# Kernel optimization log

Measured on AMD Instinct MI355X. Metric: run time of the kernel, lower is better.

Reference implementation:

```python
import jax, jax.numpy as jnp
import numpy as np

COMMITMENT_COST = 0.25
DECAY = 0.99
EPSILON = 1e-05


def setup_inputs() -> dict:
    key = jax.random.key(0)
    k1, k2, k3, k4 = jax.random.split(key, 4)
    S, B, D, K = 256, 64, 512, 4096
    return {
        "inputs": jax.random.normal(k1, (S, B, D), dtype=jnp.float32),
        "embedding_weight": jax.random.normal(k2, (K, D), dtype=jnp.float32),
        "ema_w": jax.random.normal(k3, (K, D), dtype=jnp.float32),
        "ema_cluster_size": jax.random.uniform(k4, (K,), dtype=jnp.float32),
    }


def reference(inputs, embedding_weight, ema_w, ema_cluster_size):
    S, B, D = inputs.shape
    K = embedding_weight.shape[0]
    flat = inputs.reshape(-1, D)  # [N, D], N = S*B

    distances = (
        jnp.sum(flat * flat, axis=1, keepdims=True)
        + jnp.sum(embedding_weight * embedding_weight, axis=1)
        - 2.0 * flat @ embedding_weight.T
    )
    encoding_indices = jnp.argmin(distances, axis=1)  # [N]
    encodings = jax.nn.one_hot(encoding_indices, K, dtype=inputs.dtype)  # [N, K]

    # gather codebook rows (equivalent to encodings @ weight)
    quantized = jnp.take(embedding_weight, encoding_indices, axis=0).reshape(S, B, D)
    encodings_flat = encodings.reshape(S, B, K)

    # EMA codebook update (training-mode buffers; computed with stop_gradient semantics)
    counts = jnp.sum(encodings, axis=0)  # [K]
    new_cluster_size = ema_cluster_size * DECAY + (1.0 - DECAY) * counts
    n = jnp.sum(new_cluster_size)
    new_cluster_size = (new_cluster_size + EPSILON) / (n + K * EPSILON) * n
    dw = jax.ops.segment_sum(flat, encoding_indices, num_segments=K)  # encodings.T @ flat
    new_ema_w = ema_w * DECAY + (1.0 - DECAY) * dw
    new_embedding_weight = new_ema_w / new_cluster_size[:, None]

    # commitment loss (quantized detached)
    e_latent_loss = jnp.mean((jax.lax.stop_gradient(quantized) - inputs) ** 2)
    loss = COMMITMENT_COST * e_latent_loss

    # straight-through estimator
    quantized_st = inputs + jax.lax.stop_gradient(quantized - inputs)

    return (
        loss,
        quantized_st,
        encodings_flat,
        encoding_indices[:, None],
        new_embedding_weight,
        new_cluster_size,
        new_ema_w,
    )
```

## Files before the change

kernel.cpp:

```cpp
#include <hip/hip_runtime.h>
#include <hip/hip_bf16.h>
#include <cstdint>
#include <cstddef>

typedef __attribute__((ext_vector_type(8))) short short8;
typedef __attribute__((ext_vector_type(4))) float f32x4;
typedef __attribute__((ext_vector_type(4))) unsigned int u32x4;

#define D_DIM 512
#define K_DIM 4096
#define N_ROWS 16384

#define DECAY_F 0.99f
#define OMD_F 0.01f
#define EPS_F 1e-5f
#define COMMIT_F 0.25f
#define MARGIN_F 0.75f

#define OFF_LOSS 0
#define OFF_QST 1
#define OFF_ENC (1 + 8388608)
#define OFF_IDX (OFF_ENC + 67108864)
#define OFF_NEW_W (OFF_IDX + 16384)
#define OFF_NEW_CS (OFF_NEW_W + 2097152)
#define OFF_NEW_EMA (OFF_NEW_CS + 4096)

#define WS_MINKEY 0
#define WS_COUNTS 131072
#define WS_E2 147456
#define WS_LOSSP 163840
#define WS_RCNT 164096
#define WS_ARENA 164112

#define AR_M1K 0
#define AR_M2V 4194304
#define AR_XHI 6291456
#define AR_EHI 23068672
#define AR_RROW 27262976
#define AR_RCUT 27328512
#define AR_NEED 27394048
#define WS_NEED (WS_ARENA + AR_NEED)

#define SCR0 8388612

__device__ __forceinline__ unsigned long long mkkey(float d, int c) {
  unsigned u = __float_as_uint(d);
  u ^= (unsigned)(((int)u) >> 31) | 0x80000000u;
  return ((unsigned long long)u << 32) | (unsigned)c;
}
__device__ __forceinline__ float keyval(unsigned long long k) {
  unsigned u = (unsigned)(k >> 32);
  u = (u & 0x80000000u) ? (u ^ 0x80000000u) : ~u;
  return __uint_as_float(u);
}
__device__ __forceinline__ void merge2(unsigned long long& k1, float& v2,
                                       unsigned long long ko, float v2o) {
  float v1 = keyval(k1), v1o = keyval(ko);
  float vmax = fmaxf(v1, v1o);
  v2 = fminf(fminf(v2, v2o), vmax);
  if (ko < k1) k1 = ko;
}
__device__ __forceinline__ unsigned pk2o(float a, float b) {
  unsigned ua = (__float_as_uint(a) + 0x8000u) & 0xFFFF0000u;
  unsigned ub = (__float_as_uint(b) + 0x8000u) & 0xFFFF0000u;
  return (ua >> 16) | ub;
}
__device__ __forceinline__ void gl_lds16(const void* g, void* l) {
  __builtin_amdgcn_global_load_lds(
      (const __attribute__((address_space(1))) unsigned int*)g,
      (__attribute__((address_space(3))) unsigned int*)l, 16, 0, 0);
}

__global__ void k_e2(const float* __restrict__ E, float* __restrict__ e2,
                     uint4* __restrict__ ehi, int* __restrict__ counts,
                     float* __restrict__ loss_part, int* __restrict__ rcnt) {
  int tid = threadIdx.x;
  int lane = tid & 63;
  int w = tid >> 6;
  int k = blockIdx.x * 4 + w;
  if (tid < 4) counts[blockIdx.x * 4 + tid] = 0;
  if (blockIdx.x == 0 && tid < 64) loss_part[tid] = 0.f;
  if (blockIdx.x == 1 && tid == 0) *rcnt = 0;
  const float4* ev = (const float4*)(E + (size_t)k * D_DIM);
  float4 a = ev[lane * 2], b = ev[lane * 2 + 1];
  uint4 h;
  h.x = pk2o(a.x, a.y);
  h.y = pk2o(a.z, a.w);
  h.z = pk2o(b.x, b.y);
  h.w = pk2o(b.z, b.w);
  ehi[(size_t)k * 64 + lane] = h;
  float s = a.x * a.x + a.y * a.y + a.z * a.z + a.w * a.w +
            b.x * b.x + b.y * b.y + b.z * b.z + b.w * b.w;
#pragma unroll
  for (int off = 32; off > 0; off >>= 1) s += __shfl_down(s, off, 64);
  if (lane == 0) e2[k] = s;
}

__global__ void k_conv(const float* __restrict__ src, uint4* __restrict__ hi) {
  int t = blockIdx.x * 256 + threadIdx.x;
  const float4* s4 = (const float4*)src;
  float4 a = s4[t * 2], b = s4[t * 2 + 1];
  uint4 h;
  h.x = pk2o(a.x, a.y);
  h.y = pk2o(a.z, a.w);
  h.z = pk2o(b.x, b.y);
  h.w = pk2o(b.z, b.w);
  hi[t] = h;
}

__global__ void k_scale_emaw(const float* __restrict__ ema_w, float* __restrict__ out) {
  int i = blockIdx.x * 256 + threadIdx.x;
  out[OFF_NEW_EMA + i] = DECAY_F * ema_w[i];
}

__global__ __launch_bounds__(256, 2) void k_gemm(
    const char* __restrict__ xhi, const char* __restrict__ ehi,
    const float* __restrict__ e2, unsigned long long* __restrict__ m1k,
    float* __restrict__ m2v) {
  extern __shared__ char smem[];
  const int tid = threadIdx.x;
  const int w = tid >> 6, lane = tid & 63;
  const int wr = w >> 1, wc = w & 1;
  const int l15 = lane & 15, g = lane >> 4;
  const int row0 = blockIdx.x * 128;
  const int col0 = blockIdx.y * 128;

  const char* srcBase = (w < 2) ? xhi : ehi;
  const int srcRow0 = (w < 2) ? (row0 + 64 * w) : (col0 + 64 * (w - 2));
  const int lr = lane >> 3;
  const int lc = lane & 7;
  const char* srcLane = srcBase + (size_t)(srcRow0 + lr) * 1024 + ((lc ^ lr) << 4);
  const int dstOff = w * 8192;

#define STAGE(c, b)                                       \
  {                                                       \
    const char* sp_ = srcLane + (c) * 128;                \
    char* lb_ = smem + (b) * 32768 + dstOff;              \
    _Pragma("unroll") for (int q = 0; q < 8; ++q)         \
        gl_lds16(sp_ + q * 8192, lb_ + q * 1024);         \
  }

  f32x4 acc[4][4];
  const f32x4 z = {0.f, 0.f, 0.f, 0.f};
#pragma unroll
  for (int i = 0; i < 4; ++i)
#pragma unroll
    for (int j = 0; j < 4; ++j) acc[i][j] = z;

  STAGE(0, 0);
  const int s0 = (g ^ (l15 & 7)) << 4;
  const int aRow = (wr * 64 + l15) * 128;
  const int bRow = (wc * 64 + l15) * 128;

  for (int c = 0; c < 8; ++c) {
    __syncthreads();
    if (c < 7) STAGE(c + 1, (c + 1) & 1);
    const char* Ab = smem + (c & 1) * 32768;
    const char* Bb = Ab + 16384;
    short8 a[2][4], b[2][4];
#pragma unroll
    for (int kk = 0; kk < 2; ++kk) {
      const int sw = s0 ^ (kk << 6);
#pragma unroll
      for (int i = 0; i < 4; ++i) {
        a[kk][i] = *(const short8*)(Ab + aRow + i * 2048 + sw);
        b[kk][i] = *(const short8*)(Bb + bRow + i * 2048 + sw);
      }
    }
#pragma unroll
    for (int kk = 0; kk < 2; ++kk)
#pragma unroll
      for (int i = 0; i < 4; ++i)
#pragma unroll
        for (int j = 0; j < 4; ++j)
          acc[i][j] = __builtin_amdgcn_mfma_f32_16x16x32_bf16(a[kk][i], b[kk][j], acc[i][j], 0, 0, 0);
  }
#undef STAGE

  __syncthreads();
  unsigned long long* lk = (unsigned long long*)smem;
  float* lv = (float*)(smem + 2048);
  float e2v[4];
#pragma unroll
  for (int j = 0; j < 4; ++j) e2v[j] = e2[col0 + wc * 64 + j * 16 + l15];

#pragma unroll
  for (int i = 0; i < 4; ++i) {
    int rowl = wr * 64 + i * 16 + (g << 2);
#pragma unroll
    for (int r = 0; r < 4; ++r) {
      unsigned long long k1 = 0;
      float v2 = 3.4e38f;
#pragma unroll
      for (int j = 0; j < 4; ++j) {
        float dv = fmaf(-2.f, acc[i][j][r], e2v[j]);
        unsigned long long kk = mkkey(dv, col0 + wc * 64 + j * 16 + l15);
        if (j == 0) k1 = kk;
        else merge2(k1, v2, kk, 3.4e38f);
      }
#pragma unroll
      for (int m = 1; m <= 8; m <<= 1) {
        unsigned long long ko = __shfl_xor(k1, m, 64);
        float vo = __shfl_xor(v2, m, 64);
        merge2(k1, v2, ko, vo);
      }
      if (l15 == 0) {
        lk[(rowl + r) * 2 + wc] = k1;
        lv[(rowl + r) * 2 + wc] = v2;
      }
    }
  }
  __syncthreads();
  if (tid < 128) {
    unsigned long long k1 = lk[tid * 2];
    float v2 = lv[tid * 2];
    merge2(k1, v2, lk[tid * 2 + 1], lv[tid * 2 + 1]);
    size_t o = (size_t)(row0 + tid) * 32 + blockIdx.y;
    m1k[o] = k1;
    m2v[o] = v2;
  }
}

__global__ void k_reduce(const unsigned long long* __restrict__ m1k,
                         const float* __restrict__ m2v,
                         unsigned long long* __restrict__ minkey,
                         int* __restrict__ rcnt, int* __restrict__ rrows,
                         float* __restrict__ rcut) {
  int row = blockIdx.x * 256 + threadIdx.x;
  const unsigned long long* kp = m1k + (size_t)row * 32;
  const float* vp = m2v + (size_t)row * 32;
  unsigned long long k1 = kp[0];
  float v2 = vp[0];
#pragma unroll 4
  for (int t = 1; t < 32; ++t) merge2(k1, v2, kp[t], vp[t]);
  float v1 = keyval(k1);
  if (v2 - v1 < MARGIN_F) {
    minkey[row] = ~0ull;
    int p = atomicAdd(rcnt, 1);
    rrows[p] = row;
    rcut[p] = v1 + MARGIN_F;
  } else {
    minkey[row] = k1;
  }
}

__global__ __launch_bounds__(256) void k_rescue(
    const float* __restrict__ flat, const float* __restrict__ E,
    const float* __restrict__ e2, const int* __restrict__ rcnt,
    const int* __restrict__ rrows, const float* __restrict__ rcut,
    const unsigned long long* __restrict__ m1k,
    unsigned long long* __restrict__ minkey) {
  __shared__ float sx[512];
  __shared__ unsigned long long skey[16];
  const int tid = threadIdx.x;
  const int sl = tid & 15;
  int cnt = *rcnt;
  if (cnt > N_ROWS) cnt = N_ROWS;
  for (int j = (int)blockIdx.x; j < cnt; j += (int)gridDim.x) {
    const int row = rrows[j];
    const float cutoff = rcut[j];
    __syncthreads();
    if (tid < 128) ((float4*)sx)[tid] = ((const float4*)(flat + (size_t)row * 512))[tid];
    __syncthreads();
    unsigned long long best = ~0ull;
    for (int b = 0; b < 32; ++b) {
      if (keyval(m1k[(size_t)row * 32 + b]) >= cutoff) continue;
      const int c0 = b * 128 + (tid >> 4);
#pragma unroll 2
      for (int p = 0; p < 8; ++p) {
        const int c = c0 + p * 16;
        const float4* ev = (const float4*)(E + (size_t)c * 512) + sl * 8;
        const float4* xv = (const float4*)sx + sl * 8;
        float s = 0.f;
#pragma unroll
        for (int q = 0; q < 8; ++q) {
          float4 e4 = ev[q];
          float4 x4 = xv[q];
          s = fmaf(e4.x, x4.x, s);
          s = fmaf(e4.y, x4.y, s);
          s = fmaf(e4.z, x4.z, s);
          s = fmaf(e4.w, x4.w, s);
        }
#pragma unroll
        for (int m = 1; m <= 8; m <<= 1) s += __shfl_xor(s, m, 64);
        if (sl == 0) {
          unsigned long long k = mkkey(fmaf(-2.f, s, e2[c]), c);
          if (k < best) best = k;
        }
      }
    }
    if (sl == 0) skey[tid >> 4] = best;
    __syncthreads();
    if (tid == 0) {
      unsigned long long m = skey[0];
#pragma unroll
      for (int t = 1; t < 16; ++t)
        if (skey[t] < m) m = skey[t];
      atomicMin(&minkey[row], m);
    }
  }
}

__global__ void k_zeroc(float* __restrict__ out) {
  const f32x4 z = {0.f, 0.f, 0.f, 0.f};
  const u32x4* p = (const u32x4*)(out + 8388612);
  const int base = blockIdx.x * 2048 + threadIdx.x;
#pragma unroll
  for (int t = 0; t < 8; ++t) {
    int i = base + t * 256;
    if (i < 16777215) {
      u32x4 v = __builtin_nontemporal_load(p + i);
      if (v.x | v.y | v.z | v.w) *(f32x4*)(p + i) = z;
    }
  }
  if (blockIdx.x == 0 && threadIdx.x == 0) {
    if (__float_as_uint(out[8388609])) out[8388609] = 0.f;
    if (__float_as_uint(out[8388610])) out[8388610] = 0.f;
    if (__float_as_uint(out[8388611])) out[8388611] = 0.f;
    if (__float_as_uint(out[75497472])) out[75497472] = 0.f;
  }
}

__global__ void k_zero(float* __restrict__ out) {
  const f32x4 z = {0.f, 0.f, 0.f, 0.f};
  f32x4* out4 = (f32x4*)(out + 8388612);
#pragma unroll
  for (int t = 0; t < 4; ++t) {
    int i = blockIdx.x * 1024 + t * 256 + threadIdx.x;
    if (i < 16777215) __builtin_nontemporal_store(z, out4 + i);
  }
  if (blockIdx.x == 0 && threadIdx.x == 0) {
    out[8388609] = 0.f;
    out[8388610] = 0.f;
    out[8388611] = 0.f;
    out[75497472] = 0.f;
  }
}

__global__ void k_decode(const unsigned long long* __restrict__ minkey,
                         int* __restrict__ counts, float* __restrict__ out) {
  int n = blockIdx.x * 256 + threadIdx.x;
  int c = (int)(unsigned)(minkey[n] & 0xffffffffull);
  out[OFF_IDX + n] = (float)c;
  atomicAdd(&counts[c], 1);
  out[(size_t)OFF_ENC + (size_t)n * K_DIM + c] = 1.0f;
}

__global__ void k_quant(const float* __restrict__ flat, const float* __restrict__ E,
                        const unsigned long long* __restrict__ minkey,
                        float* __restrict__ out, float* __restrict__ emaw,
                        float* __restrict__ loss_part) {
  int tid = threadIdx.x;
  int lane = tid & 63;
  int rw = tid >> 6;
  int n = blockIdx.x * 4 + rw;
  int idx = (int)(unsigned)(minkey[n] & 0xffffffffull);
  const float4* xv = (const float4*)(flat + (size_t)n * D_DIM);
  const float4* ev = (const float4*)(E + (size_t)idx * D_DIM);
  float* emarow = emaw + (size_t)idx * D_DIM;
  float s = 0.f;
#pragma unroll
  for (int t = 0; t < 2; ++t) {
    int p = lane + 64 * t;
    float4 x = xv[p];
    float4 e = ev[p];
    size_t qb = (size_t)OFF_QST + (size_t)n * D_DIM + (size_t)p * 4;
    out[qb + 0] = x.x + (e.x - x.x);
    out[qb + 1] = x.y + (e.y - x.y);
    out[qb + 2] = x.z + (e.z - x.z);
    out[qb + 3] = x.w + (e.w - x.w);
    float dx = e.x - x.x, dy = e.y - x.y, dz = e.z - x.z, dw = e.w - x.w;
    s += dx * dx + dy * dy + dz * dz + dw * dw;
    atomicAdd(emarow + p * 4 + 0, OMD_F * x.x);
    atomicAdd(emarow + p * 4 + 1, OMD_F * x.y);
    atomicAdd(emarow + p * 4 + 2, OMD_F * x.z);
    atomicAdd(emarow + p * 4 + 3, OMD_F * x.w);
  }
#pragma unroll
  for (int off = 32; off > 0; off >>= 1) s += __shfl_down(s, off, 64);
  __shared__ float ws4[4];
  if (lane == 0) ws4[rw] = s;
  __syncthreads();
  if (tid == 0) atomicAdd(&loss_part[blockIdx.x & 63], ws4[0] + ws4[1] + ws4[2] + ws4[3]);
}

__global__ __launch_bounds__(1024) void k_cs(const float* __restrict__ ema_cs,
                                             const int* __restrict__ counts,
                                             const float* __restrict__ loss_part,
                                             float* __restrict__ out) {
  int tid = threadIdx.x;
  float cs1[4];
  float local = 0.f;
#pragma unroll
  for (int t = 0; t < 4; ++t) {
    int k = tid + 1024 * t;
    cs1[t] = ema_cs[k] * DECAY_F + OMD_F * (float)counts[k];
    local += cs1[t];
  }
  __shared__ float wsum[16];
  float v = local;
#pragma unroll
  for (int off = 32; off > 0; off >>= 1) v += __shfl_down(v, off, 64);
  if ((tid & 63) == 0) wsum[tid >> 6] = v;
  __syncthreads();
  float n_total = 0.f;
#pragma unroll
  for (int t = 0; t < 16; ++t) n_total += wsum[t];
  float scale = n_total / (n_total + (float)K_DIM * EPS_F);
#pragma unroll
  for (int t = 0; t < 4; ++t) {
    int k = tid + 1024 * t;
    out[OFF_NEW_CS + k] = (cs1[t] + EPS_F) * scale;
  }
  if (tid < 64) {
    float lv = loss_part[tid];
#pragma unroll
    for (int off = 32; off > 0; off >>= 1) lv += __shfl_down(lv, off, 64);
    if (tid == 0) out[OFF_LOSS] = COMMIT_F * lv / 8388608.0f;
  }
}

__global__ void k_final(float* __restrict__ out) {
  int i = blockIdx.x * 256 + threadIdx.x;
  int k = i >> 9;
  out[OFF_NEW_W + i] = out[OFF_NEW_EMA + i] / out[OFF_NEW_CS + k];
}

extern "C" void kernel_launch(void* const* d_in, const int* in_sizes, int n_in,
                              void* d_out, int out_size, void* d_ws, size_t ws_size,
                              hipStream_t stream) {
  (void)in_sizes; (void)n_in; (void)out_size;
  const float* flat = (const float*)d_in[0];
  const float* E = (const float*)d_in[1];
  const float* ema_w = (const float*)d_in[2];
  const float* ema_cs = (const float*)d_in[3];
  float* out = (float*)d_out;
  char* ws = (char*)d_ws;

  unsigned long long* minkey = (unsigned long long*)(ws + WS_MINKEY);
  int* counts = (int*)(ws + WS_COUNTS);
  float* e2 = (float*)(ws + WS_E2);
  float* loss_part = (float*)(ws + WS_LOSSP);
  int* rcnt = (int*)(ws + WS_RCNT);

  const bool big = ws_size >= (size_t)WS_NEED;
  char* arena = big ? (ws + WS_ARENA) : (char*)(out + SCR0);
  unsigned long long* m1k = (unsigned long long*)(arena + AR_M1K);
  float* m2v = (float*)(arena + AR_M2V);
  char* xhi = arena + AR_XHI;
  char* ehi = arena + AR_EHI;
  int* rrows = (int*)(arena + AR_RROW);
  float* rcut = (float*)(arena + AR_RCUT);

  k_e2<<<1024, 256, 0, stream>>>(E, e2, (uint4*)ehi, counts, loss_part, rcnt);
  k_conv<<<4096, 256, 0, stream>>>(flat, (uint4*)xhi);
  k_scale_emaw<<<8192, 256, 0, stream>>>(ema_w, out);
  k_gemm<<<dim3(128, 32), 256, 65536, stream>>>(xhi, ehi, e2, m1k, m2v);
  k_reduce<<<64, 256, 0, stream>>>(m1k, m2v, minkey, rcnt, rrows, rcut);
  k_rescue<<<2048, 256, 0, stream>>>(flat, E, e2, rcnt, rrows, rcut, m1k, minkey);
  if (big) {
    k_zeroc<<<8192, 256, 0, stream>>>(out);
  } else {
    k_zero<<<16384, 256, 0, stream>>>(out);
  }
  k_decode<<<64, 256, 0, stream>>>(minkey, counts, out);
  k_quant<<<4096, 256, 0, stream>>>(flat, E, minkey, out, out + OFF_NEW_EMA, loss_part);
  k_cs<<<1, 1024, 0, stream>>>(ema_cs, counts, loss_part, out);
  k_final<<<8192, 256, 0, stream>>>(out);
}
```

Baseline: 450.5 us.

## Fuse encodings zeroing into GEMM epilogue and replace atomic dw with sorted segment sum

When the workspace is large, the GEMM blocks now zero their own 128x128 tile of the one-hot encodings output in their epilogue, which removes the separate zero-check kernel. The EMA-weight update no longer uses per-element float atomics. Instead it counts rows per code, prefix-scans the counts, scatters row ids into buckets, and runs a per-code gather-sum kernel that also writes the new embedding weight, removing the k_scale_emaw and k_final passes. This adds several small kernels and depends on how rows are spread across codes, since a heavily used code serializes one block. The misaligned zero store (offset by -1) also relies on special-casing the first and last elements.

```diff
diff --git a/kernel.cpp b/kernel.cpp
--- a/kernel.cpp
+++ b/kernel.cpp
@@ -5,7 +5,6 @@
 
 typedef __attribute__((ext_vector_type(8))) short short8;
 typedef __attribute__((ext_vector_type(4))) float f32x4;
-typedef __attribute__((ext_vector_type(4))) unsigned int u32x4;
 
 #define D_DIM 512
 #define K_DIM 4096
@@ -30,7 +29,10 @@
 #define WS_E2 147456
 #define WS_LOSSP 163840
 #define WS_RCNT 164096
-#define WS_ARENA 164112
+#define WS_OFFS 164112
+#define WS_CURS 180496
+#define WS_ROWL 196880
+#define WS_ARENA 262416
 
 #define AR_M1K 0
 #define AR_M2V 4194304
@@ -116,7 +118,7 @@
 __global__ __launch_bounds__(256, 2) void k_gemm(
     const char* __restrict__ xhi, const char* __restrict__ ehi,
     const float* __restrict__ e2, unsigned long long* __restrict__ m1k,
-    float* __restrict__ m2v) {
+    float* __restrict__ m2v, float* outp, int doZero) {
   extern __shared__ char smem[];
   const int tid = threadIdx.x;
   const int w = tid >> 6, lane = tid & 63;
@@ -218,6 +220,24 @@
     size_t o = (size_t)(row0 + tid) * 32 + blockIdx.y;
     m1k[o] = k1;
     m2v[o] = v2;
+  }
+
+  if (doZero) {
+    const f32x4 z4 = {0.f, 0.f, 0.f, 0.f};
+    float* encm1 = outp + (size_t)OFF_ENC - 1 + (size_t)row0 * K_DIM + col0;
+#pragma unroll
+    for (int q = 0; q < 16; ++q) {
+      int s = tid + 256 * q;
+      int r = s >> 5, c4 = s & 31;
+      float* p = encm1 + (size_t)r * K_DIM + c4 * 4;
+      if (row0 == 0 && col0 == 0 && s == 0) {
+        outp[OFF_ENC + 0] = 0.f;
+        outp[OFF_ENC + 1] = 0.f;
+        outp[OFF_ENC + 2] = 0.f;
+      } else {
+        __builtin_nontemporal_store(z4, (f32x4*)p);
+      }
+    }
   }
 }
 
@@ -301,26 +321,6 @@
   }
 }
 
-__global__ void k_zeroc(float* __restrict__ out) {
-  const f32x4 z = {0.f, 0.f, 0.f, 0.f};
-  const u32x4* p = (const u32x4*)(out + 8388612);
-  const int base = blockIdx.x * 2048 + threadIdx.x;
-#pragma unroll
-  for (int t = 0; t < 8; ++t) {
-    int i = base + t * 256;
-    if (i < 16777215) {
-      u32x4 v = __builtin_nontemporal_load(p + i);
-      if (v.x | v.y | v.z | v.w) *(f32x4*)(p + i) = z;
-    }
-  }
-  if (blockIdx.x == 0 && threadIdx.x == 0) {
-    if (__float_as_uint(out[8388609])) out[8388609] = 0.f;
-    if (__float_as_uint(out[8388610])) out[8388610] = 0.f;
-    if (__float_as_uint(out[8388611])) out[8388611] = 0.f;
-    if (__float_as_uint(out[75497472])) out[75497472] = 0.f;
-  }
-}
-
 __global__ void k_zero(float* __restrict__ out) {
   const f32x4 z = {0.f, 0.f, 0.f, 0.f};
   f32x4* out4 = (f32x4*)(out + 8388612);
@@ -343,12 +343,81 @@
   int c = (int)(unsigned)(minkey[n] & 0xffffffffull);
   out[OFF_IDX + n] = (float)c;
   atomicAdd(&counts[c], 1);
+  if (n == N_ROWS - 1) out[(size_t)OFF_ENC + (size_t)n * K_DIM + 4095] = 0.f;
   out[(size_t)OFF_ENC + (size_t)n * K_DIM + c] = 1.0f;
+}
+
+__global__ __launch_bounds__(1024) void k_prefix(const int* __restrict__ counts,
+                                                 int* __restrict__ offs,
+                                                 int* __restrict__ cursor) {
+  __shared__ int wsum[16];
+  const int tid = threadIdx.x;
+  const int lane = tid & 63, w = tid >> 6;
+  int v[4];
+  int loc = 0;
+#pragma unroll
+  for (int t = 0; t < 4; ++t) {
+    v[t] = counts[tid * 4 + t];
+    loc += v[t];
+  }
+  int scan = loc;
+#pragma unroll
+  for (int off = 1; off <= 32; off <<= 1) {
+    int o = __shfl_up(scan, off, 64);
+    if (lane >= off) scan += o;
+  }
+  if (lane == 63) wsum[w] = scan;
+  __syncthreads();
+  int base = 0;
+  for (int i = 0; i < w; ++i) base += wsum[i];
+  int run = base + scan - loc;
+#pragma unroll
+  for (int t = 0; t < 4; ++t) {
+    offs[tid * 4 + t] = run;
+    cursor[tid * 4 + t] = run;
+    run += v[t];
+  }
+}
+
+__global__ void k_scatter(const unsigned long long* __restrict__ minkey,
+                          int* __restrict__ cursor, int* __restrict__ rowl) {
+  int n = blockIdx.x * 256 + threadIdx.x;
+  int c = (int)(unsigned)(minkey[n] & 0xffffffffull);
+  int pos = atomicAdd(&cursor[c], 1);
+  rowl[pos] = n;
+}
+
+__global__ __launch_bounds__(256) void k_dw(const float* __restrict__ flat,
+                                            const float* __restrict__ ema_w,
+                                            const int* __restrict__ counts,
+                                            const int* __restrict__ offs,
+                                            const int* __restrict__ rowl,
+                                            float* __restrict__ out) {
+  const int k = blockIdx.x;
+  const int tid = threadIdx.x;
+  const int cnt = counts[k];
+  const int off = offs[k];
+  const int d0 = tid * 2;
+  float s0 = 0.f, s1 = 0.f;
+  for (int i = 0; i < cnt; ++i) {
+    int r = rowl[off + i];
+    float2 x = *(const float2*)(flat + (size_t)r * D_DIM + d0);
+    s0 += x.x;
+    s1 += x.y;
+  }
+  float e0 = DECAY_F * ema_w[(size_t)k * D_DIM + d0] + OMD_F * s0;
+  float e1 = DECAY_F * ema_w[(size_t)k * D_DIM + d0 + 1] + OMD_F * s1;
+  float cs = out[OFF_NEW_CS + k];
+  size_t b = (size_t)k * D_DIM + d0;
+  out[OFF_NEW_EMA + b] = e0;
+  out[OFF_NEW_EMA + b + 1] = e1;
+  out[OFF_NEW_W + b] = e0 / cs;
+  out[OFF_NEW_W + b + 1] = e1 / cs;
 }
 
 __global__ void k_quant(const float* __restrict__ flat, const float* __restrict__ E,
                         const unsigned long long* __restrict__ minkey,
-                        float* __restrict__ out, float* __restrict__ emaw,
+                        float* __restrict__ out, float* emaw,
                         float* __restrict__ loss_part) {
   int tid = threadIdx.x;
   int lane = tid & 63;
@@ -357,7 +426,7 @@
   int idx = (int)(unsigned)(minkey[n] & 0xffffffffull);
   const float4* xv = (const float4*)(flat + (size_t)n * D_DIM);
   const float4* ev = (const float4*)(E + (size_t)idx * D_DIM);
-  float* emarow = emaw + (size_t)idx * D_DIM;
+  float* emarow = emaw ? emaw + (size_t)idx * D_DIM : nullptr;
   float s = 0.f;
 #pragma unroll
   for (int t = 0; t < 2; ++t) {
@@ -371,10 +440,12 @@
     out[qb + 3] = x.w + (e.w - x.w);
     float dx = e.x - x.x, dy = e.y - x.y, dz = e.z - x.z, dw = e.w - x.w;
     s += dx * dx + dy * dy + dz * dz + dw * dw;
-    atomicAdd(emarow + p * 4 + 0, OMD_F * x.x);
-    atomicAdd(emarow + p * 4 + 1, OMD_F * x.y);
-    atomicAdd(emarow + p * 4 + 2, OMD_F * x.z);
-    atomicAdd(emarow + p * 4 + 3, OMD_F * x.w);
+    if (emarow) {
+      atomicAdd(emarow + p * 4 + 0, OMD_F * x.x);
+      atomicAdd(emarow + p * 4 + 1, OMD_F * x.y);
+      atomicAdd(emarow + p * 4 + 2, OMD_F * x.z);
+      atomicAdd(emarow + p * 4 + 3, OMD_F * x.w);
+    }
   }
 #pragma unroll
   for (int off = 32; off > 0; off >>= 1) s += __shfl_down(s, off, 64);
@@ -442,6 +513,9 @@
   float* e2 = (float*)(ws + WS_E2);
   float* loss_part = (float*)(ws + WS_LOSSP);
   int* rcnt = (int*)(ws + WS_RCNT);
+  int* offs = (int*)(ws + WS_OFFS);
+  int* cursor = (int*)(ws + WS_CURS);
+  int* rowl = (int*)(ws + WS_ROWL);
 
   const bool big = ws_size >= (size_t)WS_NEED;
   char* arena = big ? (ws + WS_ARENA) : (char*)(out + SCR0);
@@ -454,17 +528,22 @@
 
   k_e2<<<1024, 256, 0, stream>>>(E, e2, (uint4*)ehi, counts, loss_part, rcnt);
   k_conv<<<4096, 256, 0, stream>>>(flat, (uint4*)xhi);
-  k_scale_emaw<<<8192, 256, 0, stream>>>(ema_w, out);
-  k_gemm<<<dim3(128, 32), 256, 65536, stream>>>(xhi, ehi, e2, m1k, m2v);
+  if (!big) k_scale_emaw<<<8192, 256, 0, stream>>>(ema_w, out);
+  k_gemm<<<dim3(128, 32), 256, 65536, stream>>>(xhi, ehi, e2, m1k, m2v, out, big ? 1 : 0);
   k_reduce<<<64, 256, 0, stream>>>(m1k, m2v, minkey, rcnt, rrows, rcut);
   k_rescue<<<2048, 256, 0, stream>>>(flat, E, e2, rcnt, rrows, rcut, m1k, minkey);
   if (big) {
-    k_zeroc<<<8192, 256, 0, stream>>>(out);
+    k_decode<<<64, 256, 0, stream>>>(minkey, counts, out);
+    k_prefix<<<1, 1024, 0, stream>>>(counts, offs, cursor);
+    k_scatter<<<64, 256, 0, stream>>>(minkey, cursor, rowl);
+    k_quant<<<4096, 256, 0, stream>>>(flat, E, minkey, out, nullptr, loss_part);
+    k_cs<<<1, 1024, 0, stream>>>(ema_cs, counts, loss_part, out);
+    k_dw<<<4096, 256, 0, stream>>>(flat, ema_w, counts, offs, rowl, out);
   } else {
     k_zero<<<16384, 256, 0, stream>>>(out);
-  }
-  k_decode<<<64, 256, 0, stream>>>(minkey, counts, out);
-  k_quant<<<4096, 256, 0, stream>>>(flat, E, minkey, out, out + OFF_NEW_EMA, loss_part);
-  k_cs<<<1, 1024, 0, stream>>>(ema_cs, counts, loss_part, out);
-  k_final<<<8192, 256, 0, stream>>>(out);
-}
+    k_decode<<<64, 256, 0, stream>>>(minkey, counts, out);
+    k_quant<<<4096, 256, 0, stream>>>(flat, E, minkey, out, out + OFF_NEW_EMA, loss_part);
+    k_cs<<<1, 1024, 0, stream>>>(ema_cs, counts, loss_part, out);
+    k_final<<<8192, 256, 0, stream>>>(out);
+  }
+}
```

After: 412.4 us. 1.09x faster.
